# Performance work log

Measured on AMD Instinct MI355X. Metric: run time of the kernel, lower is better.

## Reference

```python
import jax, jax.numpy as jnp
import numpy as np

N_NODES = 50000
N_EDGES = 800000
N_GRAPHS = 64
NODE_F = 11
EDGE_F = 14
H = 128
P = 128
L = 3
BN_EPS = 1e-5


def setup_inputs() -> dict:
    key = jax.random.key(0)
    ks = jax.random.split(key, 12)
    s = lambda k, sh: (jax.random.normal(k, sh, jnp.float32) * 0.05)
    x = jax.random.normal(ks[0], (N_NODES, NODE_F), jnp.float32)
    edge_index = jax.random.randint(ks[1], (2, N_EDGES), 0, N_NODES)
    edge_attr = jax.random.normal(ks[2], (N_EDGES, EDGE_F), jnp.float32)
    batch_idx = jnp.sort(jax.random.randint(ks[3], (N_NODES,), 0, N_GRAPHS))
    node_W = s(ks[4], (H, NODE_F)); node_b = jnp.zeros((H,), jnp.float32)
    edge_W = s(ks[5], (H, EDGE_F)); edge_b = jnp.zeros((H,), jnp.float32)
    lin1_W = s(ks[6], (L, H, H)); lin1_b = jnp.zeros((L, H), jnp.float32)
    bn_gamma = jnp.ones((L, H), jnp.float32); bn_beta = jnp.zeros((L, H), jnp.float32)
    bn_mean = s(ks[7], (L, H))
    bn_var = jax.random.uniform(ks[8], (L, H), jnp.float32, 0.5, 1.5)
    lin2_W = s(ks[9], (L, H, H)); lin2_b = jnp.zeros((L, H), jnp.float32)
    proj_W = s(ks[10], (P, H)); proj_b = jnp.zeros((P,), jnp.float32)
    return dict(x=x, edge_index=edge_index, edge_attr=edge_attr, batch_idx=batch_idx,
                node_W=node_W, node_b=node_b, edge_W=edge_W, edge_b=edge_b,
                lin1_W=lin1_W, lin1_b=lin1_b, bn_gamma=bn_gamma, bn_beta=bn_beta,
                bn_mean=bn_mean, bn_var=bn_var, lin2_W=lin2_W, lin2_b=lin2_b,
                proj_W=proj_W, proj_b=proj_b)


def reference(x, edge_index, edge_attr, batch_idx, node_W, node_b, edge_W, edge_b,
              lin1_W, lin1_b, bn_gamma, bn_beta, bn_mean, bn_var,
              lin2_W, lin2_b, proj_W, proj_b):
    src, dst = edge_index[0], edge_index[1]
    h = x @ node_W.T + node_b            # [N, H] node embedding
    e = edge_attr @ edge_W.T + edge_b    # [E, H] edge embedding
    for i in range(L):
        # GINEConv: out = MLP((1+eps)*h + sum_j ReLU(h_j + e_ij)), eps = 0
        msg = jax.nn.relu(h[src] + e)                              # [E, H]
        agg = jax.ops.segment_sum(msg, dst, num_segments=N_NODES)  # [N, H]
        z = h + agg
        z = z @ lin1_W[i].T + lin1_b[i]
        # BatchNorm1d in eval mode (running stats)
        z = (z - bn_mean[i]) * (bn_gamma[i] * jax.lax.rsqrt(bn_var[i] + BN_EPS)) + bn_beta[i]
        z = jax.nn.relu(z)
        z = z @ lin2_W[i].T + lin2_b[i]
        # encoder: relu -> dropout(eval, identity) -> residual add
        h = jax.nn.relu(z) + h
    # global_mean_pool over graphs in the batch
    ones = jnp.ones((N_NODES,), h.dtype)
    counts = jax.ops.segment_sum(ones, batch_idx, num_segments=N_GRAPHS)
    pooled = jax.ops.segment_sum(h, batch_idx, num_segments=N_GRAPHS)
    pooled = pooled / jnp.maximum(counts, 1.0)[:, None]            # [G, H]
    return pooled @ proj_W.T + proj_b                              # [G, P]
```

## Files before the change

### kernel.cpp

```cpp
#include <hip/hip_runtime.h>

typedef unsigned int uint;
typedef unsigned short ushort;
typedef __attribute__((ext_vector_type(8))) short bf16x8;
typedef __attribute__((ext_vector_type(4))) float f32x4;
typedef __attribute__((ext_vector_type(2))) _Float16 half2_t;

#define NN 50000
#define NE 800000
#define NG 64
#define NODE_F 11
#define EDGE_F 14
#define HD 128
#define NL 3
#define BN_EPS 1e-5f

#if defined(__has_builtin)
#if __has_builtin(__builtin_amdgcn_fdot2)
#define HAS_DOT2 1
#endif
#endif

__device__ __forceinline__ uint bfround(float v) {
    uint b = __float_as_uint(v);
    return (b + 0x7fffu + ((b >> 16) & 1u)) >> 16;
}

__device__ __forceinline__ float dot2f(half2_t a, half2_t b, float acc) {
#ifdef HAS_DOT2
    return __builtin_amdgcn_fdot2(a, b, acc, false);
#else
    return acc + (float)a[0] * (float)b[0] + (float)a[1] * (float)b[1];
#endif
}

__device__ __forceinline__ half2_t u2h2(uint u) {
    return __builtin_bit_cast(half2_t, u);
}

__global__ __launch_bounds__(256)
void init_kernel(const float* __restrict__ x, const float* __restrict__ nW,
                 const float* __restrict__ nb_, const float* __restrict__ lin1,
                 const float* __restrict__ lin2, const float* __restrict__ proj,
                 float* __restrict__ h, uint* __restrict__ hb,
                 ushort* __restrict__ wb, float* __restrict__ projT)
{
    int bid = blockIdx.x;
    if (bid < 448) {
        int idx = bid * 256 + threadIdx.x;
        if (idx >= 7 * HD * HD) return;
        if (idx < 6 * HD * HD) {
            int m = idx >> 14, e = idx & (HD * HD - 1);
            const float* src = (m < 3) ? (lin1 + m * HD * HD) : (lin2 + (m - 3) * HD * HD);
            wb[idx] = (ushort)bfround(src[e]);
        } else {
            int e = idx - 6 * HD * HD;
            int r = e >> 7, c = e & 127;
            projT[c * HD + r] = proj[r * HD + c];
        }
    } else {
        int idx = (bid - 448) * 256 + threadIdx.x;
        if (idx >= NN * 64) return;
        int node = idx >> 6, cp = idx & 63;
        int c2 = cp * 2;
        const float* xr = x + node * NODE_F;
        const float* w0 = nW + c2 * NODE_F;
        const float* w1 = w0 + NODE_F;
        float a0 = nb_[c2], a1 = nb_[c2 + 1];
#pragma unroll
        for (int f = 0; f < NODE_F; ++f) { float xv = xr[f]; a0 += xv * w0[f]; a1 += xv * w1[f]; }
        *(float2*)&h[(size_t)node * HD + c2] = make_float2(a0, a1);
        hb[idx] = bfround(a0) | (bfround(a1) << 16);
    }
}

__global__ __launch_bounds__(256)
void hist_kernel(const int* __restrict__ ei, int* __restrict__ deg)
{
    int e = blockIdx.x * 256 + threadIdx.x;
    if (e < NE) atomicAdd(&deg[ei[NE + e]], 1);
}

__global__ __launch_bounds__(256)
void scan1_kernel(const int* __restrict__ deg, int* __restrict__ incl, int* __restrict__ bsum)
{
    int i = blockIdx.x * 256 + threadIdx.x;
    int v = (i < NN) ? deg[i] : 0;
    int lane = threadIdx.x & 63;
#pragma unroll
    for (int off = 1; off < 64; off <<= 1) {
        int u = __shfl_up(v, off);
        if (lane >= off) v += u;
    }
    __shared__ int wsum[4];
    if (lane == 63) wsum[threadIdx.x >> 6] = v;
    __syncthreads();
    int wid = threadIdx.x >> 6;
    int add = 0;
#pragma unroll
    for (int w = 0; w < 3; ++w) if (w < wid) add += wsum[w];
    v += add;
    if (i < NN) incl[i] = v;
    if (threadIdx.x == 255) bsum[blockIdx.x] = v;
}

__global__ __launch_bounds__(256)
void scan2_kernel(const int* __restrict__ bsum, int* __restrict__ bscan, int nb)
{
    int i = threadIdx.x;
    int v = (i < nb) ? bsum[i] : 0;
    int lane = i & 63;
#pragma unroll
    for (int off = 1; off < 64; off <<= 1) {
        int u = __shfl_up(v, off);
        if (lane >= off) v += u;
    }
    __shared__ int wsum[4];
    if (lane == 63) wsum[i >> 6] = v;
    __syncthreads();
    int wid = i >> 6;
    int add = 0;
#pragma unroll
    for (int w = 0; w < 3; ++w) if (w < wid) add += wsum[w];
    v += add;
    bscan[i] = v;
}

__global__ __launch_bounds__(256)
void scan3_kernel(const int* __restrict__ deg, const int* __restrict__ incl,
                  const int* __restrict__ bscan, int* __restrict__ row_start,
                  int* __restrict__ cursor)
{
    int i = blockIdx.x * 256 + threadIdx.x;
    if (i >= NN) return;
    int b = blockIdx.x;
    int base = (b > 0) ? bscan[b - 1] : 0;
    int rs = base + incl[i] - deg[i];
    row_start[i] = rs;
    cursor[i] = rs;
    if (i == 0) row_start[NN] = NE;
}

__global__ __launch_bounds__(256)
void scatter_kernel(const int* __restrict__ ei, int* __restrict__ cursor,
                    int* __restrict__ srcs, int* __restrict__ eid)
{
    int e = blockIdx.x * 256 + threadIdx.x;
    if (e >= NE) return;
    int s = ei[e], d = ei[NE + e];
    int pos = atomicAdd(&cursor[d], 1);
    srcs[pos] = s;
    eid[pos] = e;
}

__global__ __launch_bounds__(256)
void permute_f16_kernel(const float* __restrict__ ea, const int* __restrict__ eid,
                        uint* __restrict__ ea_h)
{
    int idx = blockIdx.x * 256 + threadIdx.x;
    if (idx >= NE * 8) return;
    int el = idx >> 3, f2 = idx & 7;
    if (f2 >= 7) return;
    float2 v = *(const float2*)(ea + (size_t)eid[el] * EDGE_F + 2 * f2);
    half2_t hh;
    hh[0] = (_Float16)v.x;
    hh[1] = (_Float16)v.y;
    ea_h[(size_t)el * 7 + f2] = __builtin_bit_cast(uint, hh);
}

#define EMSGH(HV, EP)                                                       \
    {                                                                       \
        float ax = bx, ay = by;                                             \
        _Pragma("unroll")                                                   \
        for (int f = 0; f < 7; ++f) {                                       \
            half2_t av = u2h2((EP)[f]);                                     \
            ax = dot2f(av, w0h[f], ax);                                     \
            ay = dot2f(av, w1h[f], ay);                                     \
        }                                                                   \
        float hx = __uint_as_float((HV) << 16);                             \
        float hy = __uint_as_float((HV) & 0xffff0000u);                     \
        accx += fmaxf(hx + ax, 0.f);                                        \
        accy += fmaxf(hy + ay, 0.f);                                        \
    }

__global__ __launch_bounds__(256)
void agg_f16_kernel(const float* __restrict__ h, const uint* __restrict__ hb,
                    const int* __restrict__ srcs, const int* __restrict__ row_start,
                    const uint* __restrict__ ea_h, const float* __restrict__ eW,
                    const float* __restrict__ eb, float* __restrict__ zin)
{
    int node = blockIdx.x * 4 + (threadIdx.x >> 6);
    if (node >= NN) return;
    int lane = threadIdx.x & 63;
    int c2 = lane * 2;
    const float4* wp = (const float4*)(eW + lane * 28);
    float4 q0 = wp[0], q1 = wp[1], q2 = wp[2], q3 = wp[3], q4 = wp[4], q5 = wp[5], q6 = wp[6];
    float w0f[14], w1f[14];
    w0f[0]=q0.x; w0f[1]=q0.y; w0f[2]=q0.z; w0f[3]=q0.w;
    w0f[4]=q1.x; w0f[5]=q1.y; w0f[6]=q1.z; w0f[7]=q1.w;
    w0f[8]=q2.x; w0f[9]=q2.y; w0f[10]=q2.z; w0f[11]=q2.w;
    w0f[12]=q3.x; w0f[13]=q3.y;
    w1f[0]=q3.z; w1f[1]=q3.w;
    w1f[2]=q4.x; w1f[3]=q4.y; w1f[4]=q4.z; w1f[5]=q4.w;
    w1f[6]=q5.x; w1f[7]=q5.y; w1f[8]=q5.z; w1f[9]=q5.w;
    w1f[10]=q6.x; w1f[11]=q6.y; w1f[12]=q6.z; w1f[13]=q6.w;
    half2_t w0h[7], w1h[7];
#pragma unroll
    for (int f = 0; f < 7; ++f) {
        w0h[f][0] = (_Float16)w0f[2 * f]; w0h[f][1] = (_Float16)w0f[2 * f + 1];
        w1h[f][0] = (_Float16)w1f[2 * f]; w1h[f][1] = (_Float16)w1f[2 * f + 1];
    }
    float bx = eb[c2], by = eb[c2 + 1];
    float accx = 0.f, accy = 0.f;
    int beg = __builtin_amdgcn_readfirstlane(row_start[node]);
    int end = __builtin_amdgcn_readfirstlane(row_start[node + 1]);
    int j = beg;
    for (; j + 8 <= end; j += 8) {
        int s[8];
        uint hv[8];
#pragma unroll
        for (int q = 0; q < 8; ++q) s[q] = srcs[j + q];
#pragma unroll
        for (int q = 0; q < 8; ++q) hv[q] = hb[(size_t)s[q] * 64 + lane];
        const uint* e0 = ea_h + (size_t)j * 7;
        EMSGH(hv[0], e0);      EMSGH(hv[1], e0 + 7);
        EMSGH(hv[2], e0 + 14); EMSGH(hv[3], e0 + 21);
        EMSGH(hv[4], e0 + 28); EMSGH(hv[5], e0 + 35);
        EMSGH(hv[6], e0 + 42); EMSGH(hv[7], e0 + 49);
    }
    for (; j + 4 <= end; j += 4) {
        int s0 = srcs[j], s1 = srcs[j + 1], s2 = srcs[j + 2], s3 = srcs[j + 3];
        uint hv0 = hb[(size_t)s0 * 64 + lane];
        uint hv1 = hb[(size_t)s1 * 64 + lane];
        uint hv2 = hb[(size_t)s2 * 64 + lane];
        uint hv3 = hb[(size_t)s3 * 64 + lane];
        const uint* e0 = ea_h + (size_t)j * 7;
        EMSGH(hv0, e0);      EMSGH(hv1, e0 + 7);
        EMSGH(hv2, e0 + 14); EMSGH(hv3, e0 + 21);
    }
    for (; j < end; ++j) {
        uint hv0 = hb[(size_t)srcs[j] * 64 + lane];
        const uint* e0 = ea_h + (size_t)j * 7;
        EMSGH(hv0, e0);
    }
    float2 hn = *(const float2*)&h[(size_t)node * HD + c2];
    *(float2*)&zin[(size_t)node * HD + c2] = make_float2(hn.x + accx, hn.y + accy);
}

__global__ __launch_bounds__(256)
void fused_layer_kernel(const float* __restrict__ zin,
                        const ushort* __restrict__ w1b, const float* __restrict__ b1,
                        const float* __restrict__ gamma, const float* __restrict__ beta,
                        const float* __restrict__ mean, const float* __restrict__ var,
                        const ushort* __restrict__ w2b, const float* __restrict__ b2,
                        float* __restrict__ h, ushort* __restrict__ hb, int n)
{
    __shared__ uint Ahi[64 * 64];
    __shared__ uint Alo[64 * 64];
    const int t = threadIdx.x;
    const int nb = blockIdx.x * 64;

    {
        int row = t >> 2;
        int kq = (t & 3) * 32;
        int gn = nb + row;
        uint hiw[16], low[16];
        if (gn < n) {
            const float4* src = (const float4*)(zin + (size_t)gn * HD + kq);
#pragma unroll
            for (int i = 0; i < 8; ++i) {
                float4 v = src[i];
                uint h0 = bfround(v.x), h1 = bfround(v.y), h2 = bfround(v.z), h3 = bfround(v.w);
                float r0 = v.x - __uint_as_float(h0 << 16);
                float r1 = v.y - __uint_as_float(h1 << 16);
                float r2 = v.z - __uint_as_float(h2 << 16);
                float r3 = v.w - __uint_as_float(h3 << 16);
                hiw[2 * i]     = h0 | (h1 << 16);
                hiw[2 * i + 1] = h2 | (h3 << 16);
                low[2 * i]     = bfround(r0) | (bfround(r1) << 16);
                low[2 * i + 1] = bfround(r2) | (bfround(r3) << 16);
            }
        } else {
#pragma unroll
            for (int i = 0; i < 16; ++i) { hiw[i] = 0; low[i] = 0; }
        }
        uint rowbase = row * 256;
#pragma unroll
        for (int i = 0; i < 4; ++i) {
            uint byte = (rowbase + (kq + 8 * i) * 2) ^ ((row & 7) << 4);
            *(uint4*)((char*)Ahi + byte) = make_uint4(hiw[4 * i], hiw[4 * i + 1], hiw[4 * i + 2], hiw[4 * i + 3]);
            *(uint4*)((char*)Alo + byte) = make_uint4(low[4 * i], low[4 * i + 1], low[4 * i + 2], low[4 * i + 3]);
        }
    }

    const int w  = t >> 6, l = t & 63;
    const int lc = l & 15, lk = l >> 4;
    bf16x8 wf1[2][4], wf2[2][4];
#pragma unroll
    for (int ct = 0; ct < 2; ++ct)
#pragma unroll
        for (int ks = 0; ks < 4; ++ks) {
            size_t off = (size_t)(w * 32 + ct * 16 + lc) * HD + ks * 32 + lk * 8;
            wf1[ct][ks] = *(const bf16x8*)(w1b + off);
            wf2[ct][ks] = *(const bf16x8*)(w2b + off);
        }

    __syncthreads();

    f32x4 acc[4][2];
#pragma unroll
    for (int rt = 0; rt < 4; ++rt)
#pragma unroll
        for (int ct = 0; ct < 2; ++ct) acc[rt][ct] = (f32x4){0.f, 0.f, 0.f, 0.f};

#pragma unroll
    for (int ks = 0; ks < 4; ++ks) {
#pragma unroll
        for (int rt = 0; rt < 4; ++rt) {
            int row = rt * 16 + lc;
            uint byte = ((uint)(row * 256 + (ks * 32 + lk * 8) * 2)) ^ ((row & 7) << 4);
            bf16x8 ah = *(const bf16x8*)((char*)Ahi + byte);
            bf16x8 al = *(const bf16x8*)((char*)Alo + byte);
            acc[rt][0] = __builtin_amdgcn_mfma_f32_16x16x32_bf16(ah, wf1[0][ks], acc[rt][0], 0, 0, 0);
            acc[rt][0] = __builtin_amdgcn_mfma_f32_16x16x32_bf16(al, wf1[0][ks], acc[rt][0], 0, 0, 0);
            acc[rt][1] = __builtin_amdgcn_mfma_f32_16x16x32_bf16(ah, wf1[1][ks], acc[rt][1], 0, 0, 0);
            acc[rt][1] = __builtin_amdgcn_mfma_f32_16x16x32_bf16(al, wf1[1][ks], acc[rt][1], 0, 0, 0);
        }
    }

    __syncthreads();

#pragma unroll
    for (int ct = 0; ct < 2; ++ct) {
        int col = w * 32 + ct * 16 + lc;
        float bi = b1[col];
        float scv = gamma[col] * rsqrtf(var[col] + BN_EPS);
        float shv = beta[col] - mean[col] * scv;
#pragma unroll
        for (int rt = 0; rt < 4; ++rt) {
#pragma unroll
            for (int r = 0; r < 4; ++r) {
                int rowl = rt * 16 + lk * 4 + r;
                float v = (acc[rt][ct][r] + bi) * scv + shv;
                v = fmaxf(v, 0.f);
                uint byte = ((uint)(rowl * 256 + col * 2)) ^ ((rowl & 7) << 4);
                *(ushort*)((char*)Ahi + byte) = (ushort)bfround(v);
            }
        }
    }

    __syncthreads();

    f32x4 acc2[4][2];
#pragma unroll
    for (int rt = 0; rt < 4; ++rt)
#pragma unroll
        for (int ct = 0; ct < 2; ++ct) acc2[rt][ct] = (f32x4){0.f, 0.f, 0.f, 0.f};

#pragma unroll
    for (int ks = 0; ks < 4; ++ks) {
#pragma unroll
        for (int rt = 0; rt < 4; ++rt) {
            int row = rt * 16 + lc;
            uint byte = ((uint)(row * 256 + (ks * 32 + lk * 8) * 2)) ^ ((row & 7) << 4);
            bf16x8 az = *(const bf16x8*)((char*)Ahi + byte);
            acc2[rt][0] = __builtin_amdgcn_mfma_f32_16x16x32_bf16(az, wf2[0][ks], acc2[rt][0], 0, 0, 0);
            acc2[rt][1] = __builtin_amdgcn_mfma_f32_16x16x32_bf16(az, wf2[1][ks], acc2[rt][1], 0, 0, 0);
        }
    }

#pragma unroll
    for (int ct = 0; ct < 2; ++ct) {
        int col = w * 32 + ct * 16 + lc;
        float bi = b2[col];
#pragma unroll
        for (int rt = 0; rt < 4; ++rt) {
#pragma unroll
            for (int r = 0; r < 4; ++r) {
                int row = nb + rt * 16 + lk * 4 + r;
                if (row < n) {
                    float v = fmaxf(acc2[rt][ct][r] + bi, 0.f) + h[(size_t)row * HD + col];
                    h[(size_t)row * HD + col] = v;
                    hb[(size_t)row * HD + col] = (ushort)bfround(v);
                }
            }
        }
    }
}

__global__ __launch_bounds__(128)
void pool_kernel(const float* __restrict__ h, const int* __restrict__ batch,
                 float* __restrict__ pooled, int* __restrict__ counts, int n, int chunk)
{
    int c = threadIdx.x;
    int n_start = blockIdx.x * chunk;
    if (n_start >= n) return;
    int n_end = min(n_start + chunk, n);
    float local = 0.f;
    int cnt = 0;
    int g_cur = batch[n_start];
    for (int nd = n_start; nd < n_end; ++nd) {
        int g = batch[nd];
        if (g != g_cur) {
            atomicAdd(&pooled[g_cur * HD + c], local);
            if (c == 0) atomicAdd(&counts[g_cur], cnt);
            local = 0.f; cnt = 0; g_cur = g;
        }
        local += h[(size_t)nd * HD + c];
        cnt++;
    }
    atomicAdd(&pooled[g_cur * HD + c], local);
    if (c == 0) atomicAdd(&counts[g_cur], cnt);
}

__global__ __launch_bounds__(128)
void final_kernel(const float* __restrict__ pooled, const int* __restrict__ counts,
                  const float* __restrict__ projT, const float* __restrict__ pb,
                  float* __restrict__ out)
{
    __shared__ float p_lds[HD];
    int g = blockIdx.x, p = threadIdx.x;
    float inv = 1.f / fmaxf((float)counts[g], 1.f);
    p_lds[p] = pooled[g * HD + p];
    __syncthreads();
    float acc = 0.f;
#pragma unroll 4
    for (int c = 0; c < HD; ++c) acc += p_lds[c] * projT[c * HD + p];
    out[g * HD + p] = acc * inv + pb[p];
}

extern "C" void kernel_launch(void* const* d_in, const int* in_sizes, int n_in,
                              void* d_out, int out_size, void* d_ws, size_t ws_size,
                              hipStream_t stream)
{
    const float* x        = (const float*)d_in[0];
    const int*   edge_idx = (const int*)d_in[1];
    const float* edge_attr= (const float*)d_in[2];
    const int*   batch    = (const int*)d_in[3];
    const float* node_W   = (const float*)d_in[4];
    const float* node_b   = (const float*)d_in[5];
    const float* edge_W   = (const float*)d_in[6];
    const float* edge_b   = (const float*)d_in[7];
    const float* lin1_b   = (const float*)d_in[9];
    const float* bn_gamma = (const float*)d_in[10];
    const float* bn_beta  = (const float*)d_in[11];
    const float* bn_mean  = (const float*)d_in[12];
    const float* bn_var   = (const float*)d_in[13];
    const float* lin2_b   = (const float*)d_in[15];
    const float* proj_b   = (const float*)d_in[17];

    char* ws = (char*)d_ws;
    float*  h        = (float*) (ws);
    float*  zin      = (float*) (ws + 25600000);
    uint*   hb       = (uint*)  (ws + 51200000);
    int*    srcs     = (int*)   (ws + 64000000);
    int*    eid      = (int*)   (ws + 67200000);
    ushort* wb       = (ushort*)(ws + 70400000);
    float*  projT    = (float*) (ws + 70600000);
    float*  pooled   = (float*) (ws + 70700000);
    int*    counts   = (int*)   (ws + 70732768);
    int*    deg      = (int*)   (ws + 70740000);
    int*    incl     = (int*)   (ws + 70940000);
    int*    bsum     = (int*)   (ws + 71140000);
    int*    bscan    = (int*)   (ws + 71142048);
    int*    row_start= (int*)   (ws + 71144096);
    int*    cursor   = (int*)   (ws + 71344160);
    uint*   ea_h     = (uint*)  (ws + 72000000);

    const int NB = (NN + 255) / 256;

    hipMemsetAsync(deg, 0, NN * sizeof(int), stream);
    hist_kernel<<<(NE + 255) / 256, 256, 0, stream>>>(edge_idx, deg);
    scan1_kernel<<<NB, 256, 0, stream>>>(deg, incl, bsum);
    scan2_kernel<<<1, 256, 0, stream>>>(bsum, bscan, NB);
    scan3_kernel<<<NB, 256, 0, stream>>>(deg, incl, bscan, row_start, cursor);
    scatter_kernel<<<(NE + 255) / 256, 256, 0, stream>>>(edge_idx, cursor, srcs, eid);
    permute_f16_kernel<<<(NE * 8 + 255) / 256, 256, 0, stream>>>(edge_attr, eid, ea_h);

    init_kernel<<<448 + (NN * 64 + 255) / 256, 256, 0, stream>>>(
        x, node_W, node_b, (const float*)d_in[8], (const float*)d_in[14],
        (const float*)d_in[16], h, hb, wb, projT);

    for (int i = 0; i < NL; ++i) {
        agg_f16_kernel<<<(NN + 3) / 4, 256, 0, stream>>>(
            h, hb, srcs, row_start, ea_h, edge_W, edge_b, zin);
        fused_layer_kernel<<<(NN + 63) / 64, 256, 0, stream>>>(
            zin, wb + (size_t)i * HD * HD, lin1_b + i * HD,
            bn_gamma + i * HD, bn_beta + i * HD, bn_mean + i * HD, bn_var + i * HD,
            wb + (size_t)(3 + i) * HD * HD, lin2_b + i * HD,
            h, (ushort*)hb, NN);
    }

    hipMemsetAsync(pooled, 0, NG * HD * sizeof(float) + NG * sizeof(int) + 4000, stream);
    pool_kernel<<<(NN + 31) / 32, 128, 0, stream>>>(h, batch, pooled, counts, NN, 32);
    final_kernel<<<NG, HD, 0, stream>>>(pooled, counts, projT, proj_b, (float*)d_out);
}
```

Before: 443.8 us.

## Fuse aggregation into layer MLP kernel and drop fp32 node state

The edge aggregation is moved into the per-layer MLP kernel, which now writes the aggregated rows straight into shared memory. This removes the fp32 zin round trip through global memory and one launch per layer. The fp32 h buffer is also dropped: the residual, self term and pooling read bf16 h from ping-pong buffers, and the edge-attribute permute is folded into the init kernel. The costs are coarser parallelism (64 nodes per block gathered serially by 4 waves, 16 nodes each), more load imbalance, and bf16 rounding of the residual stream, which changes accuracy.

```diff
diff --git a/kernel.cpp b/kernel.cpp
--- a/kernel.cpp
+++ b/kernel.cpp
@@ -42,25 +42,24 @@
 void init_kernel(const float* __restrict__ x, const float* __restrict__ nW,
                  const float* __restrict__ nb_, const float* __restrict__ lin1,
                  const float* __restrict__ lin2, const float* __restrict__ proj,
-                 float* __restrict__ h, uint* __restrict__ hb,
+                 const float* __restrict__ ea, const int* __restrict__ eid,
+                 uint* __restrict__ hb, uint* __restrict__ ea_h,
                  ushort* __restrict__ wb, float* __restrict__ projT)
 {
     int bid = blockIdx.x;
     if (bid < 448) {
         int idx = bid * 256 + threadIdx.x;
-        if (idx >= 7 * HD * HD) return;
         if (idx < 6 * HD * HD) {
             int m = idx >> 14, e = idx & (HD * HD - 1);
             const float* src = (m < 3) ? (lin1 + m * HD * HD) : (lin2 + (m - 3) * HD * HD);
             wb[idx] = (ushort)bfround(src[e]);
-        } else {
+        } else if (idx < 7 * HD * HD) {
             int e = idx - 6 * HD * HD;
             int r = e >> 7, c = e & 127;
             projT[c * HD + r] = proj[r * HD + c];
         }
-    } else {
+    } else if (bid < 448 + 12500) {
         int idx = (bid - 448) * 256 + threadIdx.x;
-        if (idx >= NN * 64) return;
         int node = idx >> 6, cp = idx & 63;
         int c2 = cp * 2;
         const float* xr = x + node * NODE_F;
@@ -69,8 +68,16 @@
         float a0 = nb_[c2], a1 = nb_[c2 + 1];
 #pragma unroll
         for (int f = 0; f < NODE_F; ++f) { float xv = xr[f]; a0 += xv * w0[f]; a1 += xv * w1[f]; }
-        *(float2*)&h[(size_t)node * HD + c2] = make_float2(a0, a1);
         hb[idx] = bfround(a0) | (bfround(a1) << 16);
+    } else {
+        int idx = (bid - 448 - 12500) * 256 + threadIdx.x;
+        int el = idx >> 3, f2 = idx & 7;
+        if (f2 >= 7) return;
+        float2 v = *(const float2*)(ea + (size_t)eid[el] * EDGE_F + 2 * f2);
+        half2_t hh;
+        hh[0] = (_Float16)v.x;
+        hh[1] = (_Float16)v.y;
+        ea_h[(size_t)el * 7 + f2] = __builtin_bit_cast(uint, hh);
     }
 }
 
@@ -151,21 +158,6 @@
     int pos = atomicAdd(&cursor[d], 1);
     srcs[pos] = s;
     eid[pos] = e;
-}
-
-__global__ __launch_bounds__(256)
-void permute_f16_kernel(const float* __restrict__ ea, const int* __restrict__ eid,
-                        uint* __restrict__ ea_h)
-{
-    int idx = blockIdx.x * 256 + threadIdx.x;
-    if (idx >= NE * 8) return;
-    int el = idx >> 3, f2 = idx & 7;
-    if (f2 >= 7) return;
-    float2 v = *(const float2*)(ea + (size_t)eid[el] * EDGE_F + 2 * f2);
-    half2_t hh;
-    hh[0] = (_Float16)v.x;
-    hh[1] = (_Float16)v.y;
-    ea_h[(size_t)el * 7 + f2] = __builtin_bit_cast(uint, hh);
 }
 
 #define EMSGH(HV, EP)                                                       \
@@ -184,117 +176,93 @@
     }
 
 __global__ __launch_bounds__(256)
-void agg_f16_kernel(const float* __restrict__ h, const uint* __restrict__ hb,
-                    const int* __restrict__ srcs, const int* __restrict__ row_start,
-                    const uint* __restrict__ ea_h, const float* __restrict__ eW,
-                    const float* __restrict__ eb, float* __restrict__ zin)
-{
-    int node = blockIdx.x * 4 + (threadIdx.x >> 6);
-    if (node >= NN) return;
-    int lane = threadIdx.x & 63;
-    int c2 = lane * 2;
-    const float4* wp = (const float4*)(eW + lane * 28);
-    float4 q0 = wp[0], q1 = wp[1], q2 = wp[2], q3 = wp[3], q4 = wp[4], q5 = wp[5], q6 = wp[6];
-    float w0f[14], w1f[14];
-    w0f[0]=q0.x; w0f[1]=q0.y; w0f[2]=q0.z; w0f[3]=q0.w;
-    w0f[4]=q1.x; w0f[5]=q1.y; w0f[6]=q1.z; w0f[7]=q1.w;
-    w0f[8]=q2.x; w0f[9]=q2.y; w0f[10]=q2.z; w0f[11]=q2.w;
-    w0f[12]=q3.x; w0f[13]=q3.y;
-    w1f[0]=q3.z; w1f[1]=q3.w;
-    w1f[2]=q4.x; w1f[3]=q4.y; w1f[4]=q4.z; w1f[5]=q4.w;
-    w1f[6]=q5.x; w1f[7]=q5.y; w1f[8]=q5.z; w1f[9]=q5.w;
-    w1f[10]=q6.x; w1f[11]=q6.y; w1f[12]=q6.z; w1f[13]=q6.w;
-    half2_t w0h[7], w1h[7];
-#pragma unroll
-    for (int f = 0; f < 7; ++f) {
-        w0h[f][0] = (_Float16)w0f[2 * f]; w0h[f][1] = (_Float16)w0f[2 * f + 1];
-        w1h[f][0] = (_Float16)w1f[2 * f]; w1h[f][1] = (_Float16)w1f[2 * f + 1];
-    }
-    float bx = eb[c2], by = eb[c2 + 1];
-    float accx = 0.f, accy = 0.f;
-    int beg = __builtin_amdgcn_readfirstlane(row_start[node]);
-    int end = __builtin_amdgcn_readfirstlane(row_start[node + 1]);
-    int j = beg;
-    for (; j + 8 <= end; j += 8) {
-        int s[8];
-        uint hv[8];
-#pragma unroll
-        for (int q = 0; q < 8; ++q) s[q] = srcs[j + q];
-#pragma unroll
-        for (int q = 0; q < 8; ++q) hv[q] = hb[(size_t)s[q] * 64 + lane];
-        const uint* e0 = ea_h + (size_t)j * 7;
-        EMSGH(hv[0], e0);      EMSGH(hv[1], e0 + 7);
-        EMSGH(hv[2], e0 + 14); EMSGH(hv[3], e0 + 21);
-        EMSGH(hv[4], e0 + 28); EMSGH(hv[5], e0 + 35);
-        EMSGH(hv[6], e0 + 42); EMSGH(hv[7], e0 + 49);
-    }
-    for (; j + 4 <= end; j += 4) {
-        int s0 = srcs[j], s1 = srcs[j + 1], s2 = srcs[j + 2], s3 = srcs[j + 3];
-        uint hv0 = hb[(size_t)s0 * 64 + lane];
-        uint hv1 = hb[(size_t)s1 * 64 + lane];
-        uint hv2 = hb[(size_t)s2 * 64 + lane];
-        uint hv3 = hb[(size_t)s3 * 64 + lane];
-        const uint* e0 = ea_h + (size_t)j * 7;
-        EMSGH(hv0, e0);      EMSGH(hv1, e0 + 7);
-        EMSGH(hv2, e0 + 14); EMSGH(hv3, e0 + 21);
-    }
-    for (; j < end; ++j) {
-        uint hv0 = hb[(size_t)srcs[j] * 64 + lane];
-        const uint* e0 = ea_h + (size_t)j * 7;
-        EMSGH(hv0, e0);
-    }
-    float2 hn = *(const float2*)&h[(size_t)node * HD + c2];
-    *(float2*)&zin[(size_t)node * HD + c2] = make_float2(hn.x + accx, hn.y + accy);
-}
-
-__global__ __launch_bounds__(256)
-void fused_layer_kernel(const float* __restrict__ zin,
-                        const ushort* __restrict__ w1b, const float* __restrict__ b1,
-                        const float* __restrict__ gamma, const float* __restrict__ beta,
-                        const float* __restrict__ mean, const float* __restrict__ var,
-                        const ushort* __restrict__ w2b, const float* __restrict__ b2,
-                        float* __restrict__ h, ushort* __restrict__ hb, int n)
+void layer_kernel(const uint* __restrict__ hb_prev,
+                  const int* __restrict__ srcs, const int* __restrict__ row_start,
+                  const uint* __restrict__ ea_h, const float* __restrict__ eW,
+                  const float* __restrict__ eb,
+                  const ushort* __restrict__ w1b, const float* __restrict__ b1,
+                  const float* __restrict__ gamma, const float* __restrict__ beta,
+                  const float* __restrict__ mean, const float* __restrict__ var,
+                  const ushort* __restrict__ w2b, const float* __restrict__ b2,
+                  ushort* __restrict__ hb_next, int n)
 {
     __shared__ uint Ahi[64 * 64];
     __shared__ uint Alo[64 * 64];
     const int t = threadIdx.x;
     const int nb = blockIdx.x * 64;
+    const int w = t >> 6, lane = t & 63;
+    const int c2 = lane * 2;
 
     {
-        int row = t >> 2;
-        int kq = (t & 3) * 32;
-        int gn = nb + row;
-        uint hiw[16], low[16];
-        if (gn < n) {
-            const float4* src = (const float4*)(zin + (size_t)gn * HD + kq);
-#pragma unroll
-            for (int i = 0; i < 8; ++i) {
-                float4 v = src[i];
-                uint h0 = bfround(v.x), h1 = bfround(v.y), h2 = bfround(v.z), h3 = bfround(v.w);
-                float r0 = v.x - __uint_as_float(h0 << 16);
-                float r1 = v.y - __uint_as_float(h1 << 16);
-                float r2 = v.z - __uint_as_float(h2 << 16);
-                float r3 = v.w - __uint_as_float(h3 << 16);
-                hiw[2 * i]     = h0 | (h1 << 16);
-                hiw[2 * i + 1] = h2 | (h3 << 16);
-                low[2 * i]     = bfround(r0) | (bfround(r1) << 16);
-                low[2 * i + 1] = bfround(r2) | (bfround(r3) << 16);
+        const float4* wp = (const float4*)(eW + lane * 28);
+        float4 q0 = wp[0], q1 = wp[1], q2 = wp[2], q3 = wp[3], q4 = wp[4], q5 = wp[5], q6 = wp[6];
+        half2_t w0h[7], w1h[7];
+        w0h[0][0]=(_Float16)q0.x; w0h[0][1]=(_Float16)q0.y;
+        w0h[1][0]=(_Float16)q0.z; w0h[1][1]=(_Float16)q0.w;
+        w0h[2][0]=(_Float16)q1.x; w0h[2][1]=(_Float16)q1.y;
+        w0h[3][0]=(_Float16)q1.z; w0h[3][1]=(_Float16)q1.w;
+        w0h[4][0]=(_Float16)q2.x; w0h[4][1]=(_Float16)q2.y;
+        w0h[5][0]=(_Float16)q2.z; w0h[5][1]=(_Float16)q2.w;
+        w0h[6][0]=(_Float16)q3.x; w0h[6][1]=(_Float16)q3.y;
+        w1h[0][0]=(_Float16)q3.z; w1h[0][1]=(_Float16)q3.w;
+        w1h[1][0]=(_Float16)q4.x; w1h[1][1]=(_Float16)q4.y;
+        w1h[2][0]=(_Float16)q4.z; w1h[2][1]=(_Float16)q4.w;
+        w1h[3][0]=(_Float16)q5.x; w1h[3][1]=(_Float16)q5.y;
+        w1h[4][0]=(_Float16)q5.z; w1h[4][1]=(_Float16)q5.w;
+        w1h[5][0]=(_Float16)q6.x; w1h[5][1]=(_Float16)q6.y;
+        w1h[6][0]=(_Float16)q6.z; w1h[6][1]=(_Float16)q6.w;
+        float bx = eb[c2], by = eb[c2 + 1];
+
+        for (int ni = 0; ni < 16; ++ni) {
+            int rowl = w * 16 + ni;
+            int node = nb + rowl;
+            float accx = 0.f, accy = 0.f;
+            if (node < n) {
+                int beg = __builtin_amdgcn_readfirstlane(row_start[node]);
+                int end = __builtin_amdgcn_readfirstlane(row_start[node + 1]);
+                int j = beg;
+                for (; j + 8 <= end; j += 8) {
+                    int s[8];
+                    uint hv[8];
+#pragma unroll
+                    for (int q = 0; q < 8; ++q) s[q] = srcs[j + q];
+#pragma unroll
+                    for (int q = 0; q < 8; ++q) hv[q] = hb_prev[(size_t)s[q] * 64 + lane];
+                    const uint* e0 = ea_h + (size_t)j * 7;
+                    EMSGH(hv[0], e0);      EMSGH(hv[1], e0 + 7);
+                    EMSGH(hv[2], e0 + 14); EMSGH(hv[3], e0 + 21);
+                    EMSGH(hv[4], e0 + 28); EMSGH(hv[5], e0 + 35);
+                    EMSGH(hv[6], e0 + 42); EMSGH(hv[7], e0 + 49);
+                }
+                for (; j + 4 <= end; j += 4) {
+                    int s0 = srcs[j], s1 = srcs[j + 1], s2 = srcs[j + 2], s3 = srcs[j + 3];
+                    uint hv0 = hb_prev[(size_t)s0 * 64 + lane];
+                    uint hv1 = hb_prev[(size_t)s1 * 64 + lane];
+                    uint hv2 = hb_prev[(size_t)s2 * 64 + lane];
+                    uint hv3 = hb_prev[(size_t)s3 * 64 + lane];
+                    const uint* e0 = ea_h + (size_t)j * 7;
+                    EMSGH(hv0, e0);      EMSGH(hv1, e0 + 7);
+                    EMSGH(hv2, e0 + 14); EMSGH(hv3, e0 + 21);
+                }
+                for (; j < end; ++j) {
+                    uint hv0 = hb_prev[(size_t)srcs[j] * 64 + lane];
+                    const uint* e0 = ea_h + (size_t)j * 7;
+                    EMSGH(hv0, e0);
+                }
+                uint hself = hb_prev[(size_t)node * 64 + lane];
+                accx += __uint_as_float(hself << 16);
+                accy += __uint_as_float(hself & 0xffff0000u);
             }
-        } else {
-#pragma unroll
-            for (int i = 0; i < 16; ++i) { hiw[i] = 0; low[i] = 0; }
-        }
-        uint rowbase = row * 256;
-#pragma unroll
-        for (int i = 0; i < 4; ++i) {
-            uint byte = (rowbase + (kq + 8 * i) * 2) ^ ((row & 7) << 4);
-            *(uint4*)((char*)Ahi + byte) = make_uint4(hiw[4 * i], hiw[4 * i + 1], hiw[4 * i + 2], hiw[4 * i + 3]);
-            *(uint4*)((char*)Alo + byte) = make_uint4(low[4 * i], low[4 * i + 1], low[4 * i + 2], low[4 * i + 3]);
-        }
-    }
-
-    const int w  = t >> 6, l = t & 63;
-    const int lc = l & 15, lk = l >> 4;
+            uint h0 = bfround(accx), h1 = bfround(accy);
+            float r0 = accx - __uint_as_float(h0 << 16);
+            float r1 = accy - __uint_as_float(h1 << 16);
+            uint byte = ((uint)(rowl * 256 + c2 * 2)) ^ ((rowl & 7) << 4);
+            *(uint*)((char*)Ahi + byte) = h0 | (h1 << 16);
+            *(uint*)((char*)Alo + byte) = bfround(r0) | (bfround(r1) << 16);
+        }
+    }
+
+    const int lc = lane & 15, lk = lane >> 4;
     bf16x8 wf1[2][4], wf2[2][4];
 #pragma unroll
     for (int ct = 0; ct < 2; ++ct)
@@ -369,6 +337,7 @@
         }
     }
 
+    const ushort* hp16 = (const ushort*)hb_prev;
 #pragma unroll
     for (int ct = 0; ct < 2; ++ct) {
         int col = w * 32 + ct * 16 + lc;
@@ -379,9 +348,9 @@
             for (int r = 0; r < 4; ++r) {
                 int row = nb + rt * 16 + lk * 4 + r;
                 if (row < n) {
-                    float v = fmaxf(acc2[rt][ct][r] + bi, 0.f) + h[(size_t)row * HD + col];
-                    h[(size_t)row * HD + col] = v;
-                    hb[(size_t)row * HD + col] = (ushort)bfround(v);
+                    float hprev = __uint_as_float(((uint)hp16[(size_t)row * HD + col]) << 16);
+                    float v = fmaxf(acc2[rt][ct][r] + bi, 0.f) + hprev;
+                    hb_next[(size_t)row * HD + col] = (ushort)bfround(v);
                 }
             }
         }
@@ -389,7 +358,7 @@
 }
 
 __global__ __launch_bounds__(128)
-void pool_kernel(const float* __restrict__ h, const int* __restrict__ batch,
+void pool_kernel(const ushort* __restrict__ hb, const int* __restrict__ batch,
                  float* __restrict__ pooled, int* __restrict__ counts, int n, int chunk)
 {
     int c = threadIdx.x;
@@ -406,7 +375,7 @@
             if (c == 0) atomicAdd(&counts[g_cur], cnt);
             local = 0.f; cnt = 0; g_cur = g;
         }
-        local += h[(size_t)nd * HD + c];
+        local += __uint_as_float(((uint)hb[(size_t)nd * HD + c]) << 16);
         cnt++;
     }
     atomicAdd(&pooled[g_cur * HD + c], local);
@@ -450,22 +419,21 @@
     const float* proj_b   = (const float*)d_in[17];
 
     char* ws = (char*)d_ws;
-    float*  h        = (float*) (ws);
-    float*  zin      = (float*) (ws + 25600000);
-    uint*   hb       = (uint*)  (ws + 51200000);
-    int*    srcs     = (int*)   (ws + 64000000);
-    int*    eid      = (int*)   (ws + 67200000);
-    ushort* wb       = (ushort*)(ws + 70400000);
-    float*  projT    = (float*) (ws + 70600000);
-    float*  pooled   = (float*) (ws + 70700000);
-    int*    counts   = (int*)   (ws + 70732768);
-    int*    deg      = (int*)   (ws + 70740000);
-    int*    incl     = (int*)   (ws + 70940000);
-    int*    bsum     = (int*)   (ws + 71140000);
-    int*    bscan    = (int*)   (ws + 71142048);
-    int*    row_start= (int*)   (ws + 71144096);
-    int*    cursor   = (int*)   (ws + 71344160);
-    uint*   ea_h     = (uint*)  (ws + 72000000);
+    uint*   hbA      = (uint*)  (ws);
+    uint*   hbB      = (uint*)  (ws + 12800000);
+    uint*   ea_h     = (uint*)  (ws + 25600000);
+    int*    srcs     = (int*)   (ws + 48000000);
+    int*    eid      = (int*)   (ws + 51200000);
+    ushort* wb       = (ushort*)(ws + 54400000);
+    float*  projT    = (float*) (ws + 54600000);
+    float*  pooled   = (float*) (ws + 54700000);
+    int*    counts   = (int*)   (ws + 54732768);
+    int*    deg      = (int*)   (ws + 54740000);
+    int*    incl     = (int*)   (ws + 54940000);
+    int*    bsum     = (int*)   (ws + 55140000);
+    int*    bscan    = (int*)   (ws + 55142048);
+    int*    row_start= (int*)   (ws + 55144096);
+    int*    cursor   = (int*)   (ws + 55344160);
 
     const int NB = (NN + 255) / 256;
 
@@ -475,23 +443,23 @@
     scan2_kernel<<<1, 256, 0, stream>>>(bsum, bscan, NB);
     scan3_kernel<<<NB, 256, 0, stream>>>(deg, incl, bscan, row_start, cursor);
     scatter_kernel<<<(NE + 255) / 256, 256, 0, stream>>>(edge_idx, cursor, srcs, eid);
-    permute_f16_kernel<<<(NE * 8 + 255) / 256, 256, 0, stream>>>(edge_attr, eid, ea_h);
-
-    init_kernel<<<448 + (NN * 64 + 255) / 256, 256, 0, stream>>>(
+
+    init_kernel<<<448 + 12500 + 25000, 256, 0, stream>>>(
         x, node_W, node_b, (const float*)d_in[8], (const float*)d_in[14],
-        (const float*)d_in[16], h, hb, wb, projT);
-
+        (const float*)d_in[16], edge_attr, eid, hbA, ea_h, wb, projT);
+
+    uint* prev = hbA; uint* next = hbB;
     for (int i = 0; i < NL; ++i) {
-        agg_f16_kernel<<<(NN + 3) / 4, 256, 0, stream>>>(
-            h, hb, srcs, row_start, ea_h, edge_W, edge_b, zin);
-        fused_layer_kernel<<<(NN + 63) / 64, 256, 0, stream>>>(
-            zin, wb + (size_t)i * HD * HD, lin1_b + i * HD,
+        layer_kernel<<<(NN + 63) / 64, 256, 0, stream>>>(
+            prev, srcs, row_start, ea_h, edge_W, edge_b,
+            wb + (size_t)i * HD * HD, lin1_b + i * HD,
             bn_gamma + i * HD, bn_beta + i * HD, bn_mean + i * HD, bn_var + i * HD,
             wb + (size_t)(3 + i) * HD * HD, lin2_b + i * HD,
-            h, (ushort*)hb, NN);
+            (ushort*)next, NN);
+        uint* tmp = prev; prev = next; next = tmp;
     }
 
     hipMemsetAsync(pooled, 0, NG * HD * sizeof(float) + NG * sizeof(int) + 4000, stream);
-    pool_kernel<<<(NN + 31) / 32, 128, 0, stream>>>(h, batch, pooled, counts, NN, 32);
+    pool_kernel<<<(NN + 31) / 32, 128, 0, stream>>>((const ushort*)prev, batch, pooled, counts, NN, 32);
     final_kernel<<<NG, HD, 0, stream>>>(pooled, counts, projT, proj_b, (float*)d_out);
 }
```

Result: slower. 620.0 us (+39.7%).

## Drop fp32 node state; keep only bf16 h and fuse edge permute into init

Applied to the files above, without the earlier changes.

Removes the fp32 copy of the node features entirely. The self term in aggregation, the residual add in the fused layer, and pooling now all read the bf16 buffer, and the fp32 write-back is gone. The edge-attribute permute/convert kernel is merged into the init kernel as an extra block range, which saves one launch. This cuts global memory traffic per layer, but the residual path now accumulates in bf16 across layers, which costs precision.

```diff
diff --git a/kernel.cpp b/kernel.cpp
--- a/kernel.cpp
+++ b/kernel.cpp
@@ -42,25 +42,24 @@
 void init_kernel(const float* __restrict__ x, const float* __restrict__ nW,
                  const float* __restrict__ nb_, const float* __restrict__ lin1,
                  const float* __restrict__ lin2, const float* __restrict__ proj,
-                 float* __restrict__ h, uint* __restrict__ hb,
+                 const float* __restrict__ ea, const int* __restrict__ eid,
+                 uint* __restrict__ hb, uint* __restrict__ ea_h,
                  ushort* __restrict__ wb, float* __restrict__ projT)
 {
     int bid = blockIdx.x;
     if (bid < 448) {
         int idx = bid * 256 + threadIdx.x;
-        if (idx >= 7 * HD * HD) return;
         if (idx < 6 * HD * HD) {
             int m = idx >> 14, e = idx & (HD * HD - 1);
             const float* src = (m < 3) ? (lin1 + m * HD * HD) : (lin2 + (m - 3) * HD * HD);
             wb[idx] = (ushort)bfround(src[e]);
-        } else {
+        } else if (idx < 7 * HD * HD) {
             int e = idx - 6 * HD * HD;
             int r = e >> 7, c = e & 127;
             projT[c * HD + r] = proj[r * HD + c];
         }
-    } else {
+    } else if (bid < 448 + 12500) {
         int idx = (bid - 448) * 256 + threadIdx.x;
-        if (idx >= NN * 64) return;
         int node = idx >> 6, cp = idx & 63;
         int c2 = cp * 2;
         const float* xr = x + node * NODE_F;
@@ -69,8 +68,16 @@
         float a0 = nb_[c2], a1 = nb_[c2 + 1];
 #pragma unroll
         for (int f = 0; f < NODE_F; ++f) { float xv = xr[f]; a0 += xv * w0[f]; a1 += xv * w1[f]; }
-        *(float2*)&h[(size_t)node * HD + c2] = make_float2(a0, a1);
         hb[idx] = bfround(a0) | (bfround(a1) << 16);
+    } else {
+        int idx = (bid - 448 - 12500) * 256 + threadIdx.x;
+        int el = idx >> 3, f2 = idx & 7;
+        if (f2 >= 7) return;
+        float2 v = *(const float2*)(ea + (size_t)eid[el] * EDGE_F + 2 * f2);
+        half2_t hh;
+        hh[0] = (_Float16)v.x;
+        hh[1] = (_Float16)v.y;
+        ea_h[(size_t)el * 7 + f2] = __builtin_bit_cast(uint, hh);
     }
 }
 
@@ -151,21 +158,6 @@
     int pos = atomicAdd(&cursor[d], 1);
     srcs[pos] = s;
     eid[pos] = e;
-}
-
-__global__ __launch_bounds__(256)
-void permute_f16_kernel(const float* __restrict__ ea, const int* __restrict__ eid,
-                        uint* __restrict__ ea_h)
-{
-    int idx = blockIdx.x * 256 + threadIdx.x;
-    if (idx >= NE * 8) return;
-    int el = idx >> 3, f2 = idx & 7;
-    if (f2 >= 7) return;
-    float2 v = *(const float2*)(ea + (size_t)eid[el] * EDGE_F + 2 * f2);
-    half2_t hh;
-    hh[0] = (_Float16)v.x;
-    hh[1] = (_Float16)v.y;
-    ea_h[(size_t)el * 7 + f2] = __builtin_bit_cast(uint, hh);
 }
 
 #define EMSGH(HV, EP)                                                       \
@@ -184,7 +176,7 @@
     }
 
 __global__ __launch_bounds__(256)
-void agg_f16_kernel(const float* __restrict__ h, const uint* __restrict__ hb,
+void agg_f16_kernel(const uint* __restrict__ hb,
                     const int* __restrict__ srcs, const int* __restrict__ row_start,
                     const uint* __restrict__ ea_h, const float* __restrict__ eW,
                     const float* __restrict__ eb, float* __restrict__ zin)
@@ -195,21 +187,21 @@
     int c2 = lane * 2;
     const float4* wp = (const float4*)(eW + lane * 28);
     float4 q0 = wp[0], q1 = wp[1], q2 = wp[2], q3 = wp[3], q4 = wp[4], q5 = wp[5], q6 = wp[6];
-    float w0f[14], w1f[14];
-    w0f[0]=q0.x; w0f[1]=q0.y; w0f[2]=q0.z; w0f[3]=q0.w;
-    w0f[4]=q1.x; w0f[5]=q1.y; w0f[6]=q1.z; w0f[7]=q1.w;
-    w0f[8]=q2.x; w0f[9]=q2.y; w0f[10]=q2.z; w0f[11]=q2.w;
-    w0f[12]=q3.x; w0f[13]=q3.y;
-    w1f[0]=q3.z; w1f[1]=q3.w;
-    w1f[2]=q4.x; w1f[3]=q4.y; w1f[4]=q4.z; w1f[5]=q4.w;
-    w1f[6]=q5.x; w1f[7]=q5.y; w1f[8]=q5.z; w1f[9]=q5.w;
-    w1f[10]=q6.x; w1f[11]=q6.y; w1f[12]=q6.z; w1f[13]=q6.w;
     half2_t w0h[7], w1h[7];
-#pragma unroll
-    for (int f = 0; f < 7; ++f) {
-        w0h[f][0] = (_Float16)w0f[2 * f]; w0h[f][1] = (_Float16)w0f[2 * f + 1];
-        w1h[f][0] = (_Float16)w1f[2 * f]; w1h[f][1] = (_Float16)w1f[2 * f + 1];
-    }
+    w0h[0][0]=(_Float16)q0.x; w0h[0][1]=(_Float16)q0.y;
+    w0h[1][0]=(_Float16)q0.z; w0h[1][1]=(_Float16)q0.w;
+    w0h[2][0]=(_Float16)q1.x; w0h[2][1]=(_Float16)q1.y;
+    w0h[3][0]=(_Float16)q1.z; w0h[3][1]=(_Float16)q1.w;
+    w0h[4][0]=(_Float16)q2.x; w0h[4][1]=(_Float16)q2.y;
+    w0h[5][0]=(_Float16)q2.z; w0h[5][1]=(_Float16)q2.w;
+    w0h[6][0]=(_Float16)q3.x; w0h[6][1]=(_Float16)q3.y;
+    w1h[0][0]=(_Float16)q3.z; w1h[0][1]=(_Float16)q3.w;
+    w1h[1][0]=(_Float16)q4.x; w1h[1][1]=(_Float16)q4.y;
+    w1h[2][0]=(_Float16)q4.z; w1h[2][1]=(_Float16)q4.w;
+    w1h[3][0]=(_Float16)q5.x; w1h[3][1]=(_Float16)q5.y;
+    w1h[4][0]=(_Float16)q5.z; w1h[4][1]=(_Float16)q5.w;
+    w1h[5][0]=(_Float16)q6.x; w1h[5][1]=(_Float16)q6.y;
+    w1h[6][0]=(_Float16)q6.z; w1h[6][1]=(_Float16)q6.w;
     float bx = eb[c2], by = eb[c2 + 1];
     float accx = 0.f, accy = 0.f;
     int beg = __builtin_amdgcn_readfirstlane(row_start[node]);
@@ -243,8 +235,10 @@
         const uint* e0 = ea_h + (size_t)j * 7;
         EMSGH(hv0, e0);
     }
-    float2 hn = *(const float2*)&h[(size_t)node * HD + c2];
-    *(float2*)&zin[(size_t)node * HD + c2] = make_float2(hn.x + accx, hn.y + accy);
+    uint hself = hb[(size_t)node * 64 + lane];
+    accx += __uint_as_float(hself << 16);
+    accy += __uint_as_float(hself & 0xffff0000u);
+    *(float2*)&zin[(size_t)node * HD + c2] = make_float2(accx, accy);
 }
 
 __global__ __launch_bounds__(256)
@@ -253,7 +247,7 @@
                         const float* __restrict__ gamma, const float* __restrict__ beta,
                         const float* __restrict__ mean, const float* __restrict__ var,
                         const ushort* __restrict__ w2b, const float* __restrict__ b2,
-                        float* __restrict__ h, ushort* __restrict__ hb, int n)
+                        ushort* __restrict__ hb, int n)
 {
     __shared__ uint Ahi[64 * 64];
     __shared__ uint Alo[64 * 64];
@@ -379,8 +373,8 @@
             for (int r = 0; r < 4; ++r) {
                 int row = nb + rt * 16 + lk * 4 + r;
                 if (row < n) {
-                    float v = fmaxf(acc2[rt][ct][r] + bi, 0.f) + h[(size_t)row * HD + col];
-                    h[(size_t)row * HD + col] = v;
+                    float hprev = __uint_as_float(((uint)hb[(size_t)row * HD + col]) << 16);
+                    float v = fmaxf(acc2[rt][ct][r] + bi, 0.f) + hprev;
                     hb[(size_t)row * HD + col] = (ushort)bfround(v);
                 }
             }
@@ -389,7 +383,7 @@
 }
 
 __global__ __launch_bounds__(128)
-void pool_kernel(const float* __restrict__ h, const int* __restrict__ batch,
+void pool_kernel(const ushort* __restrict__ hb, const int* __restrict__ batch,
                  float* __restrict__ pooled, int* __restrict__ counts, int n, int chunk)
 {
     int c = threadIdx.x;
@@ -406,7 +400,7 @@
             if (c == 0) atomicAdd(&counts[g_cur], cnt);
             local = 0.f; cnt = 0; g_cur = g;
         }
-        local += h[(size_t)nd * HD + c];
+        local += __uint_as_float(((uint)hb[(size_t)nd * HD + c]) << 16);
         cnt++;
     }
     atomicAdd(&pooled[g_cur * HD + c], local);
@@ -450,22 +444,21 @@
     const float* proj_b   = (const float*)d_in[17];
 
     char* ws = (char*)d_ws;
-    float*  h        = (float*) (ws);
-    float*  zin      = (float*) (ws + 25600000);
-    uint*   hb       = (uint*)  (ws + 51200000);
-    int*    srcs     = (int*)   (ws + 64000000);
-    int*    eid      = (int*)   (ws + 67200000);
-    ushort* wb       = (ushort*)(ws + 70400000);
-    float*  projT    = (float*) (ws + 70600000);
-    float*  pooled   = (float*) (ws + 70700000);
-    int*    counts   = (int*)   (ws + 70732768);
-    int*    deg      = (int*)   (ws + 70740000);
-    int*    incl     = (int*)   (ws + 70940000);
-    int*    bsum     = (int*)   (ws + 71140000);
-    int*    bscan    = (int*)   (ws + 71142048);
-    int*    row_start= (int*)   (ws + 71144096);
-    int*    cursor   = (int*)   (ws + 71344160);
-    uint*   ea_h     = (uint*)  (ws + 72000000);
+    uint*   hb       = (uint*)  (ws);
+    float*  zin      = (float*) (ws + 12800000);
+    uint*   ea_h     = (uint*)  (ws + 38400000);
+    int*    srcs     = (int*)   (ws + 60800000);
+    int*    eid      = (int*)   (ws + 64000000);
+    ushort* wb       = (ushort*)(ws + 67200000);
+    float*  projT    = (float*) (ws + 67400000);
+    float*  pooled   = (float*) (ws + 67500000);
+    int*    counts   = (int*)   (ws + 67532768);
+    int*    deg      = (int*)   (ws + 67540000);
+    int*    incl     = (int*)   (ws + 67740000);
+    int*    bsum     = (int*)   (ws + 67940000);
+    int*    bscan    = (int*)   (ws + 67942048);
+    int*    row_start= (int*)   (ws + 67944096);
+    int*    cursor   = (int*)   (ws + 68144160);
 
     const int NB = (NN + 255) / 256;
 
@@ -475,23 +468,22 @@
     scan2_kernel<<<1, 256, 0, stream>>>(bsum, bscan, NB);
     scan3_kernel<<<NB, 256, 0, stream>>>(deg, incl, bscan, row_start, cursor);
     scatter_kernel<<<(NE + 255) / 256, 256, 0, stream>>>(edge_idx, cursor, srcs, eid);
-    permute_f16_kernel<<<(NE * 8 + 255) / 256, 256, 0, stream>>>(edge_attr, eid, ea_h);
-
-    init_kernel<<<448 + (NN * 64 + 255) / 256, 256, 0, stream>>>(
+
+    init_kernel<<<448 + 12500 + 25000, 256, 0, stream>>>(
         x, node_W, node_b, (const float*)d_in[8], (const float*)d_in[14],
-        (const float*)d_in[16], h, hb, wb, projT);
+        (const float*)d_in[16], edge_attr, eid, hb, ea_h, wb, projT);
 
     for (int i = 0; i < NL; ++i) {
         agg_f16_kernel<<<(NN + 3) / 4, 256, 0, stream>>>(
-            h, hb, srcs, row_start, ea_h, edge_W, edge_b, zin);
+            hb, srcs, row_start, ea_h, edge_W, edge_b, zin);
         fused_layer_kernel<<<(NN + 63) / 64, 256, 0, stream>>>(
             zin, wb + (size_t)i * HD * HD, lin1_b + i * HD,
             bn_gamma + i * HD, bn_beta + i * HD, bn_mean + i * HD, bn_var + i * HD,
             wb + (size_t)(3 + i) * HD * HD, lin2_b + i * HD,
-            h, (ushort*)hb, NN);
+            (ushort*)hb, NN);
     }
 
     hipMemsetAsync(pooled, 0, NG * HD * sizeof(float) + NG * sizeof(int) + 4000, stream);
-    pool_kernel<<<(NN + 31) / 32, 128, 0, stream>>>(h, batch, pooled, counts, NN, 32);
+    pool_kernel<<<(NN + 31) / 32, 128, 0, stream>>>((const ushort*)hb, batch, pooled, counts, NN, 32);
     final_kernel<<<NG, HD, 0, stream>>>(pooled, counts, projT, proj_b, (float*)d_out);
 }
```

Measured after the change: 431.7 us. 1.03x faster.
